# Performance work log

Hardware: AMD Instinct MI355X
Metric: run time of the kernel (lower is better)

The kernel has to match this reference:

```python
import jax, jax.numpy as jnp
import numpy as np
from jax.scipy.special import logsumexp

SIZE = 68          # DP length (self.size)
SSN = 8            # number of secondary-structure classes
C = SSN + 1        # states per step
S1 = SIZE + 1      # positions
BATCH = 256


def setup_inputs() -> dict:
    key = jax.random.key(0)
    k1, k2, k3, k4 = jax.random.split(key, 4)
    P = jax.random.normal(k1, (BATCH, 1, C, S1, S1), jnp.float32)
    Q = jax.random.normal(k2, (1, C, C, S1, S1), jnp.float32)
    pi = jax.random.normal(k3, (C,), jnp.float32)
    T = jnp.ones((1,), jnp.float32)
    ls = jax.random.randint(k4, (BATCH,), 0, S1, dtype=jnp.int32)
    return {"P": P, "Q": Q, "pi": pi, "T": T, "ls": ls}


def _max_alpha(P, Q, pi, T):
    # Viterbi-style max-plus recursion with logsumexp renormalization.
    b = P.shape[0]
    a0 = jnp.full((b, C, S1), -jnp.inf, P.dtype).at[:, :, 0].set(pi[None, :])
    n0 = logsumexp(a0, axis=(-1, -2), keepdims=True)      # (b,1,1)
    a0 = a0 - n0

    def step(carry, _):
        la, ln = carry                                    # (b,C,S1), (b,1,1)
        # broadcast sum over (b, c_prev, c_new, t_prev, t_new)
        M = P + T * Q + la[:, :, None, :, None]
        a = M.max(axis=(1, 3))                            # max over c_prev, t_prev -> (b,C,S1)
        n = ln + logsumexp(a, axis=(-1, -2), keepdims=True)
        a = a + ln - n
        return (a, n), (a, n)

    _, (a_seq, n_seq) = jax.lax.scan(step, (a0, n0), None, length=SIZE)
    a_all = jnp.concatenate([a0[None], a_seq], 0)          # (S1, b, C, S1) forward order
    n_all = jnp.concatenate([n0[None], n_seq], 0)          # (S1, b, 1, 1)
    # torch code stacks alpha REVERSED but norm in forward order, then adds
    alpha = a_all[::-1] + n_all
    return jnp.swapaxes(alpha, 0, 1)                       # (b, SIZE+1, C, S1)


def _backtrace(alpha, P, Q, T, ls):
    b = alpha.shape[0]
    Ps = P[:, 0]            # (b, C, S1, S1)
    Qs = Q[0]               # (C, C, S1, S1)
    bi = jnp.arange(b)
    c0 = jnp.full((b,), 3, jnp.int32)
    l0 = jnp.zeros((b,), jnp.int32)
    t0 = ls.astype(jnp.int32)

    def step(carry, a):
        c, l, t = carry
        Pterm = Ps[bi, c, :, t]                 # (b, S1)
        Qterm = Qs[c, :, :, t]                  # (b, C, S1)
        score = Pterm[:, None, :] + T * Qterm + a
        idx = jnp.argmax(score.reshape(b, -1), axis=-1).astype(jnp.int32)
        cn = idx // S1
        tn = idx % S1
        ln = tn - t
        return (cn, ln, tn), (cn, ln, tn)

    a_seq = jnp.swapaxes(alpha, 0, 1)[1:]       # (SIZE, b, C, S1)
    _, (cs, lss, ts) = jax.lax.scan(step, (c0, l0, t0), a_seq)
    c_all = jnp.concatenate([c0[None], cs], 0)[::-1]   # (SIZE+1, b)
    l_all = jnp.concatenate([l0[None], lss], 0)[::-1]
    t_all = jnp.concatenate([t0[None], ts], 0)[::-1]
    mp = jnp.swapaxes(jnp.stack([c_all, l_all, t_all], -1), 0, 1)  # (b, SIZE+1, 3)
    # shift length column: mp[:, :-1, 1] = mp[:, 1:, 1]; mp[:, -1, 1] = 0
    l_shift = jnp.concatenate([mp[:, 1:, 1], jnp.zeros((b, 1), jnp.int32)], 1)
    return mp.at[:, :, 1].set(l_shift)


def reference(P, Q, pi, T, ls):
    alpha = _max_alpha(P, Q, pi, T)
    max_pattern = _backtrace(alpha, P, Q, T, ls)
    return alpha, max_pattern
```

## Files before the change

### kernel.cpp

```cpp
#include <hip/hip_runtime.h>

#define C9     9
#define S1     69
#define JT     621
#define NBATCH 256
#define NSTEP  68
#define QJ     4761
#define QI     42849
#define BROW   42849
#define ALPHA_N (NBATCH*BROW)
#define QTFL   385664
#define NEGINF (-__builtin_inff())

typedef float float2u __attribute__((ext_vector_type(2), aligned(4)));

__global__ void qw_kernel(const float* __restrict__ Q, float* __restrict__ QW)
{
  const int bl = blockIdx.x;
  const int j = bl / S1, s = bl - j*S1;
  float* dst = QW + (size_t)bl*JT;
  const float* src = Q + (size_t)j*QJ + s*S1;
  for (int f = threadIdx.x; f < JT; f += 256){
    const int i = f / S1, t = f - i*S1;
    dst[f] = src[i*QJ + t];
  }
}

__global__ void qtrans_kernel(const float* __restrict__ Q, float* __restrict__ QT)
{
  __shared__ float tile[69*70];
  const int pl = blockIdx.x;
  const int c = pl / 9, i = pl - c*9;
  const float* src = Q + (size_t)pl*QJ;
  for (int f = threadIdx.x; f < QJ; f += 256){
    const int s = f / S1, t = f - s*S1;
    tile[s*70 + t] = src[f];
  }
  __syncthreads();
  float* dst = QT + (size_t)c*QI + i*S1;
  for (int f = threadIdx.x; f < QJ; f += 256){
    const int t = f / S1, s = f - t*S1;
    dst[t*JT + s] = tile[s*70 + t];
  }
}

template<int SI, int SS>
__device__ __forceinline__ float2u scan23(const float* __restrict__ qb,
                                          const float* __restrict__ pb,
                                          const float* __restrict__ laS,
                                          const float Tv)
{
#define LD(QB, S) { \
  const float* q_ = qb + (S)*SS; \
  _Pragma("unroll") \
  for (int i_ = 0; i_ < C9; ++i_) QB[i_] = *(const float2u*)(q_ + i_*SI); }
#define CM(QB, S) { \
  const float2u pv_ = *(const float2u*)(pb + (S)*S1); \
  float r0 = NEGINF, r1 = NEGINF; \
  _Pragma("unroll") \
  for (int i_ = 0; i_ < C9; ++i_){ \
    const float lv_ = laS[i_*72 + (S)]; \
    r0 = fmaxf(r0, fmaf(Tv, QB[i_].x, lv_)); \
    r1 = fmaxf(r1, fmaf(Tv, QB[i_].y, lv_)); \
  } \
  acc.x = fmaxf(acc.x, pv_.x + r0); \
  acc.y = fmaxf(acc.y, pv_.y + r1); }

  float2u acc; acc.x = acc.y = NEGINF;
  float2u qA[C9], qB[C9];
  LD(qA, 0)
  int s = 0;
  for (; s + 2 < 23; s += 2){
    LD(qB, s+1)
    CM(qA, s)
    LD(qA, s+2)
    CM(qB, s+1)
  }
  CM(qA, 22)
  return acc;
#undef LD
#undef CM
}

__global__ __launch_bounds__(1024) void mega_kernel(
    const float* __restrict__ P, const float* __restrict__ Q,
    const float* __restrict__ pi, const float* __restrict__ Tp,
    const int* __restrict__ ls, float* __restrict__ out,
    const float* __restrict__ QW, const float* __restrict__ QT, int wsmode)
{
  __shared__ __align__(16) float la[2][C9*72];
  __shared__ float part[2][315][3];
  __shared__ float red[16];
  __shared__ float m_sh[NSTEP+1], lse_sh[NSTEP+1], n_sh[NSTEP+1];
  __shared__ float sums_sh[NSTEP+1][5];
  __shared__ float sbest[16];
  __shared__ int   sidx[16];
  __shared__ int   sct[2];

  const int tid  = threadIdx.x;
  const int w    = tid >> 6;
  const int lane = tid & 63;
  const int b    = blockIdx.x;
  const bool act = tid < 945;
  const int gg   = act ? tid / 315 : 2;
  const int slot = act ? tid - gg*315 : 314;
  const int j    = slot / 35;
  const int tp   = slot - j*35;
  const bool own2 = (tp < 34);
  const int t0   = own2 ? 2*tp : 67;
  const int s_lo = gg*23;
  const float Tv = Tp[0];

  float* outb = out + (size_t)b*BROW;

  for (int e = tid; e < JT; e += 1024){
    const int i = e / S1, s = e - i*S1;
    const float v0 = (s == 0) ? pi[i] : NEGINF;
    outb[68*JT + e] = v0;
    la[0][i*72 + s] = v0;
  }
  if (tid == 0){
    float mx = pi[0];
    #pragma unroll
    for (int c = 1; c < C9; ++c) mx = fmaxf(mx, pi[c]);
    float sm = 0.f;
    #pragma unroll
    for (int c = 0; c < C9; ++c) sm += expf(pi[c] - mx);
    m_sh[0]   = mx;
    lse_sh[0] = mx + logf(sm);
  }
  __syncthreads();
  float mprev = m_sh[0];

  const bool useQW = (wsmode >= 1);
  const float* qw_b = QW + (size_t)j*QI + (size_t)s_lo*JT + t0;
  const float* qr_b = Q + (size_t)j*QJ + s_lo*S1 + t0;
  const float* p_b  = P + (size_t)(b*C9 + j)*QJ + s_lo*S1 + t0;

  int cur = 0;
  for (int k = 1; k <= NSTEP; ++k){
    const float* laS = la[cur] + s_lo;
    float2u acc;
    if (act){
      if (useQW) acc = scan23<S1, JT>(qw_b, p_b, laS, Tv);
      else       acc = scan23<QI, S1>(qr_b, p_b, laS, Tv);
      if (gg > 0){
        part[gg-1][slot][0] = acc.x;
        part[gg-1][slot][1] = acc.y;
      }
    }
    __syncthreads();

    float mval = NEGINF;
    float v0 = 0.f, v1 = 0.f;
    if (act && gg == 0){
      const float c0 = fmaxf(fmaxf(acc.x, part[0][slot][0]), part[1][slot][0]);
      const float c1 = fmaxf(fmaxf(acc.y, part[0][slot][1]), part[1][slot][1]);
      v0 = c0 - mprev;
      v1 = c1 - mprev;
      float* dst = outb + (size_t)(68-k)*JT + j*S1 + t0;
      if (own2){
        float2u vv; vv.x = v0; vv.y = v1;
        *(float2u*)dst = vv;
        la[cur^1][j*72 + t0]     = v0;
        la[cur^1][j*72 + t0 + 1] = v1;
        mval = fmaxf(v0, v1);
      } else {
        dst[1] = v1;
        la[cur^1][j*72 + 68] = v1;
        mval = v1;
      }
    }
    float mr = mval;
    #pragma unroll
    for (int o = 32; o >= 1; o >>= 1) mr = fmaxf(mr, __shfl_down(mr, o));
    if (lane == 0) red[w] = mr;
    __syncthreads();
    float mA = red[0];
    #pragma unroll
    for (int q = 1; q < 5; ++q) mA = fmaxf(mA, red[q]);
    if (act && gg == 0){
      float sv = own2 ? (expf(v0 - mA) + expf(v1 - mA)) : expf(v1 - mA);
      #pragma unroll
      for (int o = 32; o >= 1; o >>= 1) sv += __shfl_down(sv, o);
      if (lane == 0) sums_sh[k][w] = sv;
    }
    if (tid == 0) m_sh[k] = mA;
    mprev = mA;
    cur ^= 1;
  }
  __syncthreads();

  if (tid == 0){
    double dd = 0.0;
    for (int kk = 0; kk <= NSTEP; ++kk){
      float lse;
      if (kk == 0) lse = lse_sh[0];
      else {
        float S = sums_sh[kk][0];
        #pragma unroll
        for (int q = 1; q < 5; ++q) S += sums_sh[kk][q];
        lse = m_sh[kk] + logf(S);
      }
      lse_sh[kk] = lse;
      n_sh[kk] = (float)((double)lse + dd);
      dd += (double)m_sh[kk];
    }
  }
  __syncthreads();

  for (int K = 0; K <= NSTEP; ++K){
    const float Cst = n_sh[K] - lse_sh[68-K];
    for (int e = tid; e < JT; e += 1024){
      float* r = outb + (size_t)K*JT + e;
      *r = fmaxf(*r + Cst, -3.0e38f);
    }
  }
  __syncthreads();

  {
    int c = 3, t2 = ls[b];
    float* mpb = out + (size_t)ALPHA_N + (size_t)b*(69*3);
    if (tid == 0){
      mpb[68*3+0] = 3.f; mpb[68*3+1] = 0.f; mpb[68*3+2] = (float)t2;
      mpb[67*3+1] = 0.f;
    }
    const bool vok = tid < JT;
    const int etid = vok ? tid : 0;
    const int im = etid / S1;
    const int sm = etid - im*S1;
    float av = vok ? outb[1*JT + tid] : NEGINF;
    for (int r = 1; r <= NSTEP; ++r){
      float avn = NEGINF;
      if (r < NSTEP && vok) avn = outb[(size_t)(r+1)*JT + tid];
      float best = NEGINF; int bidx = 0x7fffffff;
      if (vok){
        float qv;
        if (wsmode >= 2)      qv = QT[(size_t)c*QI + (size_t)t2*JT + tid];
        else if (wsmode == 1) qv = QW[(size_t)c*QI + (size_t)sm*JT + im*S1 + t2];
        else                  qv = Q[(size_t)c*QI + (size_t)im*QJ + sm*S1 + t2];
        const float pv = P[(size_t)(b*C9 + c)*QJ + sm*S1 + t2];
        best = (pv + Tv*qv) + av;
        bidx = tid;
      }
      #pragma unroll
      for (int o = 32; o >= 1; o >>= 1){
        const float ov = __shfl_down(best, o); const int oi = __shfl_down(bidx, o);
        if (ov > best || (ov == best && oi < bidx)){ best = ov; bidx = oi; }
      }
      if (lane == 0){ sbest[w] = best; sidx[w] = bidx; }
      __syncthreads();
      if (tid == 0){
        float bb = sbest[0]; int bi = sidx[0];
        #pragma unroll
        for (int q = 1; q < 16; ++q)
          if (sbest[q] > bb || (sbest[q] == bb && sidx[q] < bi)){
            bb = sbest[q]; bi = sidx[q];
          }
        const int cn = bi / S1, tn = bi - cn*S1;
        mpb[(68-r)*3 + 0] = (float)cn;
        mpb[(68-r)*3 + 2] = (float)tn;
        if (r <= 67) mpb[(67-r)*3 + 1] = (float)(tn - t2);
        sct[0] = cn; sct[1] = tn;
      }
      __syncthreads();
      c = sct[0]; t2 = sct[1];
      av = avn;
    }
  }
}

extern "C" void kernel_launch(void* const* d_in, const int* in_sizes, int n_in,
                              void* d_out, int out_size, void* d_ws, size_t ws_size,
                              hipStream_t stream)
{
  const float* P  = (const float*)d_in[0];
  const float* Q  = (const float*)d_in[1];
  const float* pi = (const float*)d_in[2];
  const float* T  = (const float*)d_in[3];
  const int*   ls = (const int*)d_in[4];

  float* out = (float*)d_out;

  int wsmode = 0; float* QW = nullptr; float* QT = nullptr;
  if (ws_size >= (size_t)QTFL*4){ wsmode = 1; QW = (float*)d_ws; }
  if (ws_size >= (size_t)2*QTFL*4){ wsmode = 2; QT = (float*)d_ws + QTFL; }

  if (wsmode >= 1) qw_kernel<<<JT, 256, 0, stream>>>(Q, QW);
  if (wsmode >= 2) qtrans_kernel<<<81, 256, 0, stream>>>(Q, QT);
  mega_kernel<<<NBATCH, 1024, 0, stream>>>(P, Q, pi, T, ls, out, QW, QT, wsmode);
}
```

Before: 2.058 ms.

## Split DP scan over two thread groups and prefetch Q across steps

Each block now uses 704 threads, and the scan over previous positions is split into two groups of 35 positions instead of three groups of 23, so only one partial result buffer is merged per step. The step loop is unrolled by two with ping-pong register buffers, so the first Q slice for the next step is loaded before the barrier. A custom barrier waits only on LDS counters (lgkmcnt), letting global loads stay in flight across it. In exchange, each thread does a longer serial inner loop and the block has fewer waves to hide latency.

```diff
diff --git a/kernel.cpp b/kernel.cpp
--- a/kernel.cpp
+++ b/kernel.cpp
@@ -14,6 +14,14 @@
 
 typedef float float2u __attribute__((ext_vector_type(2), aligned(4)));
 
+__device__ __forceinline__ void barrier_lgkm()
+{
+  __builtin_amdgcn_sched_barrier(0);
+  asm volatile("s_waitcnt lgkmcnt(0)" ::: "memory");
+  __builtin_amdgcn_s_barrier();
+  __builtin_amdgcn_sched_barrier(0);
+}
+
 __global__ void qw_kernel(const float* __restrict__ Q, float* __restrict__ QW)
 {
   const int bl = blockIdx.x;
@@ -44,80 +52,42 @@
   }
 }
 
-template<int SI, int SS>
-__device__ __forceinline__ float2u scan23(const float* __restrict__ qb,
-                                          const float* __restrict__ pb,
-                                          const float* __restrict__ laS,
-                                          const float Tv)
-{
-#define LD(QB, S) { \
-  const float* q_ = qb + (S)*SS; \
-  _Pragma("unroll") \
-  for (int i_ = 0; i_ < C9; ++i_) QB[i_] = *(const float2u*)(q_ + i_*SI); }
-#define CM(QB, S) { \
-  const float2u pv_ = *(const float2u*)(pb + (S)*S1); \
-  float r0 = NEGINF, r1 = NEGINF; \
-  _Pragma("unroll") \
-  for (int i_ = 0; i_ < C9; ++i_){ \
-    const float lv_ = laS[i_*72 + (S)]; \
-    r0 = fmaxf(r0, fmaf(Tv, QB[i_].x, lv_)); \
-    r1 = fmaxf(r1, fmaf(Tv, QB[i_].y, lv_)); \
-  } \
-  acc.x = fmaxf(acc.x, pv_.x + r0); \
-  acc.y = fmaxf(acc.y, pv_.y + r1); }
-
-  float2u acc; acc.x = acc.y = NEGINF;
-  float2u qA[C9], qB[C9];
-  LD(qA, 0)
-  int s = 0;
-  for (; s + 2 < 23; s += 2){
-    LD(qB, s+1)
-    CM(qA, s)
-    LD(qA, s+2)
-    CM(qB, s+1)
-  }
-  CM(qA, 22)
-  return acc;
-#undef LD
-#undef CM
-}
-
-__global__ __launch_bounds__(1024) void mega_kernel(
+__global__ __launch_bounds__(704) void mega_kernel(
     const float* __restrict__ P, const float* __restrict__ Q,
     const float* __restrict__ pi, const float* __restrict__ Tp,
     const int* __restrict__ ls, float* __restrict__ out,
     const float* __restrict__ QW, const float* __restrict__ QT, int wsmode)
 {
   __shared__ __align__(16) float la[2][C9*72];
-  __shared__ float part[2][315][3];
-  __shared__ float red[16];
+  __shared__ float part[315][3];
+  __shared__ float red[11];
   __shared__ float m_sh[NSTEP+1], lse_sh[NSTEP+1], n_sh[NSTEP+1];
   __shared__ float sums_sh[NSTEP+1][5];
-  __shared__ float sbest[16];
-  __shared__ int   sidx[16];
+  __shared__ float sbest[11];
+  __shared__ int   sidx[11];
   __shared__ int   sct[2];
 
   const int tid  = threadIdx.x;
   const int w    = tid >> 6;
   const int lane = tid & 63;
   const int b    = blockIdx.x;
-  const bool act = tid < 945;
-  const int gg   = act ? tid / 315 : 2;
+  const bool act = tid < 630;
+  const int gg   = act ? tid / 315 : 1;
   const int slot = act ? tid - gg*315 : 314;
   const int j    = slot / 35;
   const int tp   = slot - j*35;
   const bool own2 = (tp < 34);
   const int t0   = own2 ? 2*tp : 67;
-  const int s_lo = gg*23;
+  const int s_lo = gg*34;
   const float Tv = Tp[0];
 
   float* outb = out + (size_t)b*BROW;
 
-  for (int e = tid; e < JT; e += 1024){
+  for (int e = tid; e < JT; e += 704){
     const int i = e / S1, s = e - i*S1;
-    const float v0 = (s == 0) ? pi[i] : NEGINF;
-    outb[68*JT + e] = v0;
-    la[0][i*72 + s] = v0;
+    const float v0i = (s == 0) ? pi[i] : NEGINF;
+    outb[68*JT + e] = v0i;
+    la[0][i*72 + s] = v0i;
   }
   if (tid == 0){
     float mx = pi[0];
@@ -133,62 +103,92 @@
   float mprev = m_sh[0];
 
   const bool useQW = (wsmode >= 1);
-  const float* qw_b = QW + (size_t)j*QI + (size_t)s_lo*JT + t0;
-  const float* qr_b = Q + (size_t)j*QJ + s_lo*S1 + t0;
-  const float* p_b  = P + (size_t)(b*C9 + j)*QJ + s_lo*S1 + t0;
-
-  int cur = 0;
-  for (int k = 1; k <= NSTEP; ++k){
-    const float* laS = la[cur] + s_lo;
-    float2u acc;
-    if (act){
-      if (useQW) acc = scan23<S1, JT>(qw_b, p_b, laS, Tv);
-      else       acc = scan23<QI, S1>(qr_b, p_b, laS, Tv);
-      if (gg > 0){
-        part[gg-1][slot][0] = acc.x;
-        part[gg-1][slot][1] = acc.y;
-      }
-    }
-    __syncthreads();
-
-    float mval = NEGINF;
-    float v0 = 0.f, v1 = 0.f;
-    if (act && gg == 0){
-      const float c0 = fmaxf(fmaxf(acc.x, part[0][slot][0]), part[1][slot][0]);
-      const float c1 = fmaxf(fmaxf(acc.y, part[0][slot][1]), part[1][slot][1]);
-      v0 = c0 - mprev;
-      v1 = c1 - mprev;
-      float* dst = outb + (size_t)(68-k)*JT + j*S1 + t0;
-      if (own2){
-        float2u vv; vv.x = v0; vv.y = v1;
-        *(float2u*)dst = vv;
-        la[cur^1][j*72 + t0]     = v0;
-        la[cur^1][j*72 + t0 + 1] = v1;
-        mval = fmaxf(v0, v1);
-      } else {
-        dst[1] = v1;
-        la[cur^1][j*72 + 68] = v1;
-        mval = v1;
-      }
-    }
-    float mr = mval;
-    #pragma unroll
-    for (int o = 32; o >= 1; o >>= 1) mr = fmaxf(mr, __shfl_down(mr, o));
-    if (lane == 0) red[w] = mr;
-    __syncthreads();
-    float mA = red[0];
-    #pragma unroll
-    for (int q = 1; q < 5; ++q) mA = fmaxf(mA, red[q]);
-    if (act && gg == 0){
-      float sv = own2 ? (expf(v0 - mA) + expf(v1 - mA)) : expf(v1 - mA);
-      #pragma unroll
-      for (int o = 32; o >= 1; o >>= 1) sv += __shfl_down(sv, o);
-      if (lane == 0) sums_sh[k][w] = sv;
-    }
-    if (tid == 0) m_sh[k] = mA;
-    mprev = mA;
-    cur ^= 1;
-  }
+  const float* qb = useQW ? (QW + (size_t)j*QI + (size_t)s_lo*JT + t0)
+                          : (Q  + (size_t)j*QJ + s_lo*S1 + t0);
+  const float* pb = P + (size_t)(b*C9 + j)*QJ + s_lo*S1 + t0;
+  float* la0 = la[0];
+  float* la1 = la[1];
+
+#define LDQ(B, PTR, SI) { \
+  _Pragma("unroll") \
+  for (int i_ = 0; i_ < C9; ++i_) B[i_] = *(const float2u*)((PTR) + i_*(SI)); }
+
+#define CMQ(B, PPTR, LC, IDX) { \
+  const float2u pv_ = *(const float2u*)(PPTR); \
+  float r0 = NEGINF, r1 = NEGINF; \
+  _Pragma("unroll") \
+  for (int i_ = 0; i_ < C9; ++i_){ \
+    const float lv_ = (LC)[i_*72 + (IDX)]; \
+    r0 = fmaxf(r0, fmaf(Tv, B[i_].x, lv_)); \
+    r1 = fmaxf(r1, fmaf(Tv, B[i_].y, lv_)); \
+  } \
+  acc.x = fmaxf(acc.x, pv_.x + r0); \
+  acc.y = fmaxf(acc.y, pv_.y + r1); }
+
+#define STEP(K, BE, BO, LAR, LAW, SI, SS) { \
+  float2u acc; acc.x = acc.y = NEGINF; \
+  if (act){ \
+    const float* qc = qb + (SS); \
+    const float* pc = pb; \
+    const float* lc = (LAR) + s_lo; \
+    for (int p_ = 0; p_ < 17; ++p_){ \
+      LDQ(BO, qc, SI) \
+      CMQ(BE, pc, lc, 0) \
+      LDQ(BE, qc + (SS), SI) \
+      CMQ(BO, pc + S1, lc, 1) \
+      qc += 2*(SS); pc += 2*S1; lc += 2; \
+    } \
+    LDQ(BO, qb, SI)                        \
+    CMQ(BE, pc, lc, 0)                     \
+    if (gg == 1){ part[slot][0] = acc.x; part[slot][1] = acc.y; } \
+  } \
+  barrier_lgkm();                          \
+  float mval = NEGINF; float v0 = 0.f, v1 = 0.f; \
+  if (act && gg == 0){ \
+    const float c0 = fmaxf(acc.x, part[slot][0]); \
+    const float c1 = fmaxf(acc.y, part[slot][1]); \
+    v0 = c0 - mprev; v1 = c1 - mprev; \
+    float* dst = outb + (size_t)(68-(K))*JT + j*S1 + t0; \
+    if (own2){ \
+      float2u vv; vv.x = v0; vv.y = v1; \
+      *(float2u*)dst = vv; \
+      (LAW)[j*72 + t0]     = v0; \
+      (LAW)[j*72 + t0 + 1] = v1; \
+      mval = fmaxf(v0, v1); \
+    } else { \
+      dst[1] = v1; \
+      (LAW)[j*72 + 68] = v1; \
+      mval = v1; \
+    } \
+  } \
+  float mr = mval; \
+  _Pragma("unroll") \
+  for (int o_ = 32; o_ >= 1; o_ >>= 1) mr = fmaxf(mr, __shfl_down(mr, o_)); \
+  if (lane == 0) red[w] = mr; \
+  barrier_lgkm();                          \
+  float mA = red[0]; \
+  _Pragma("unroll") \
+  for (int q_ = 1; q_ < 5; ++q_) mA = fmaxf(mA, red[q_]); \
+  float sv = 0.f; \
+  if (act && gg == 0) \
+    sv = own2 ? (expf(v0 - mA) + expf(v1 - mA)) : expf(v1 - mA); \
+  _Pragma("unroll") \
+  for (int o_ = 32; o_ >= 1; o_ >>= 1) sv += __shfl_down(sv, o_); \
+  if (lane == 0 && w < 5) sums_sh[K][w] = sv; \
+  if (tid == 0) m_sh[K] = mA; \
+  mprev = mA; }
+
+#define KLOOP(SI, SS) { \
+  float2u qE[C9], qO[C9]; \
+  if (act) LDQ(qE, qb, SI) \
+  for (int kk = 1; kk <= NSTEP; kk += 2){ \
+    STEP(kk,   qE, qO, la0, la1, SI, SS) \
+    STEP(kk+1, qO, qE, la1, la0, SI, SS) \
+  } }
+
+  if (useQW){ KLOOP(S1, JT) }
+  else      { KLOOP(QI, S1) }
+
   __syncthreads();
 
   if (tid == 0){
@@ -211,7 +211,7 @@
 
   for (int K = 0; K <= NSTEP; ++K){
     const float Cst = n_sh[K] - lse_sh[68-K];
-    for (int e = tid; e < JT; e += 1024){
+    for (int e = tid; e < JT; e += 704){
       float* r = outb + (size_t)K*JT + e;
       *r = fmaxf(*r + Cst, -3.0e38f);
     }
@@ -253,7 +253,7 @@
       if (tid == 0){
         float bb = sbest[0]; int bi = sidx[0];
         #pragma unroll
-        for (int q = 1; q < 16; ++q)
+        for (int q = 1; q < 11; ++q)
           if (sbest[q] > bb || (sbest[q] == bb && sidx[q] < bi)){
             bb = sbest[q]; bi = sidx[q];
           }
@@ -288,5 +288,5 @@
 
   if (wsmode >= 1) qw_kernel<<<JT, 256, 0, stream>>>(Q, QW);
   if (wsmode >= 2) qtrans_kernel<<<81, 256, 0, stream>>>(Q, QT);
-  mega_kernel<<<NBATCH, 1024, 0, stream>>>(P, Q, pi, T, ls, out, QW, QT, wsmode);
-}
+  mega_kernel<<<NBATCH, 704, 0, stream>>>(P, Q, pi, T, ls, out, QW, QT, wsmode);
+}
```

After: 2.111 ms. 1.03x slower.

## Split each 4-batch group across 4 cooperating blocks with global-memory step exchange

Applied to the files above, without the earlier changes.

The forward max-plus recursion is reorganized so that each group of 4 blocks handles 4 batch elements jointly. Each block owns a slice of the output time positions for all 4 batches, so every Q load is reused across 4 batches. The blocks exchange per-step column results and maxima through a global scratch buffer, synchronized with atomic flag counters and spin-waits. A fallback kernel with 704 threads covers the case of small workspace, and barriers now wait only on LDS counters. The aim is to cut per-block Q traffic and shorten the serial work per step. In exchange there is inter-block spin synchronization every step, which depends on all 4 blocks of a group being resident at the same time.

```diff
diff --git a/kernel.cpp b/kernel.cpp
--- a/kernel.cpp
+++ b/kernel.cpp
@@ -10,9 +10,23 @@
 #define BROW   42849
 #define ALPHA_N (NBATCH*BROW)
 #define QTFL   385664
+#define XCSTR  672
+#define XCFL   (64*2*4*XCSTR)
+#define FLAGN  4608
 #define NEGINF (-__builtin_inff())
 
-typedef float float2u __attribute__((ext_vector_type(2), aligned(4)));
+typedef float float2u  __attribute__((ext_vector_type(2), aligned(4)));
+typedef float float4a  __attribute__((ext_vector_type(4), aligned(16)));
+
+#define AGENT __HIP_MEMORY_SCOPE_AGENT
+
+__device__ __forceinline__ void barrier_lgkm()
+{
+  __builtin_amdgcn_sched_barrier(0);
+  asm volatile("s_waitcnt lgkmcnt(0)" ::: "memory");
+  __builtin_amdgcn_s_barrier();
+  __builtin_amdgcn_sched_barrier(0);
+}
 
 __global__ void qw_kernel(const float* __restrict__ Q, float* __restrict__ QW)
 {
@@ -44,80 +58,61 @@
   }
 }
 
-template<int SI, int SS>
-__device__ __forceinline__ float2u scan23(const float* __restrict__ qb,
-                                          const float* __restrict__ pb,
-                                          const float* __restrict__ laS,
-                                          const float Tv)
+__global__ void zf_kernel(unsigned* __restrict__ f)
 {
-#define LD(QB, S) { \
-  const float* q_ = qb + (S)*SS; \
-  _Pragma("unroll") \
-  for (int i_ = 0; i_ < C9; ++i_) QB[i_] = *(const float2u*)(q_ + i_*SI); }
-#define CM(QB, S) { \
-  const float2u pv_ = *(const float2u*)(pb + (S)*S1); \
-  float r0 = NEGINF, r1 = NEGINF; \
-  _Pragma("unroll") \
-  for (int i_ = 0; i_ < C9; ++i_){ \
-    const float lv_ = laS[i_*72 + (S)]; \
-    r0 = fmaxf(r0, fmaf(Tv, QB[i_].x, lv_)); \
-    r1 = fmaxf(r1, fmaf(Tv, QB[i_].y, lv_)); \
-  } \
-  acc.x = fmaxf(acc.x, pv_.x + r0); \
-  acc.y = fmaxf(acc.y, pv_.y + r1); }
-
-  float2u acc; acc.x = acc.y = NEGINF;
-  float2u qA[C9], qB[C9];
-  LD(qA, 0)
-  int s = 0;
-  for (; s + 2 < 23; s += 2){
-    LD(qB, s+1)
-    CM(qA, s)
-    LD(qA, s+2)
-    CM(qB, s+1)
-  }
-  CM(qA, 22)
-  return acc;
-#undef LD
-#undef CM
+  const int i = blockIdx.x*256 + threadIdx.x;
+  if (i < FLAGN) __hip_atomic_store(&f[i], 0u, __ATOMIC_RELAXED, AGENT);
 }
 
-__global__ __launch_bounds__(1024) void mega_kernel(
+__global__ __launch_bounds__(704) void mega_group(
     const float* __restrict__ P, const float* __restrict__ Q,
     const float* __restrict__ pi, const float* __restrict__ Tp,
     const int* __restrict__ ls, float* __restrict__ out,
-    const float* __restrict__ QW, const float* __restrict__ QT, int wsmode)
+    const float* __restrict__ QW, const float* __restrict__ QT,
+    float* __restrict__ XC, unsigned* __restrict__ FLAGS, int qtmode)
 {
-  __shared__ __align__(16) float la[2][C9*72];
-  __shared__ float part[2][315][3];
-  __shared__ float red[16];
-  __shared__ float m_sh[NSTEP+1], lse_sh[NSTEP+1], n_sh[NSTEP+1];
-  __shared__ float sums_sh[NSTEP+1][5];
-  __shared__ float sbest[16];
-  __shared__ int   sidx[16];
+  __shared__ __align__(16) float la4[C9*70*4];
+  __shared__ __align__(16) float part[7][81][8];
+  __shared__ float cbuf[4][624];
+  __shared__ float msh[NSTEP+1][4];
+  __shared__ float sums_sh[NSTEP+1][11][4];
+  __shared__ float mpart[2][4];
+  __shared__ float lse_sh[NSTEP+1], n_sh[NSTEP+1];
+  __shared__ float lse0_sh;
+  __shared__ float sbest[11];
+  __shared__ int   sidx[11];
   __shared__ int   sct[2];
 
   const int tid  = threadIdx.x;
-  const int w    = tid >> 6;
-  const int lane = tid & 63;
-  const int b    = blockIdx.x;
-  const bool act = tid < 945;
-  const int gg   = act ? tid / 315 : 2;
-  const int slot = act ? tid - gg*315 : 314;
-  const int j    = slot / 35;
-  const int tp   = slot - j*35;
-  const bool own2 = (tp < 34);
-  const int t0   = own2 ? 2*tp : 67;
-  const int s_lo = gg*23;
+  const int w    = tid >> 6, lane = tid & 63;
+  const int g    = blockIdx.x >> 2, h = blockIdx.x & 3;
+  const int Th   = h ? 17 : 18;
+  const int Bh   = h ? (18 + 17*(h-1)) : 0;
+  const bool act = tid < 648;
+  const int sg   = act ? tid / 81 : 7;
+  const int slot = act ? tid - sg*81 : 80;
+  const int j    = slot / 9;
+  const int tp   = slot - j*9;
+  const bool own2 = (2*tp + 1 < Th);
+  const int tl0  = own2 ? 2*tp : (Th-2);
+  const int tg0  = Bh + tl0;
+  const int Ws   = (sg < 7) ? 9 : 6;
+  const int s_lo = sg*9;
   const float Tv = Tp[0];
-
-  float* outb = out + (size_t)b*BROW;
-
-  for (int e = tid; e < JT; e += 1024){
-    const int i = e / S1, s = e - i*S1;
-    const float v0 = (s == 0) ? pi[i] : NEGINF;
-    outb[68*JT + e] = v0;
-    la[0][i*72 + s] = v0;
+  const int bb   = 4*g + h;
+  unsigned* flg  = FLAGS + g*72;
+
+  for (int e = tid; e < JT; e += 704){
+    const int ii = e / 69, ss = e - ii*69;
+    const float v0 = (ss == 0) ? pi[ii] : NEGINF;
+    float4a vv; vv.x = vv.y = vv.z = vv.w = v0;
+    *(float4a*)(&la4[(ii*70 + ss)*4]) = vv;
+  }
+  for (int idx = tid; idx < 4*9*Th; idx += 704){
+    const int m = idx / (9*Th); const int rem = idx - m*(9*Th);
+    const int jj = rem / Th;    const int tl = rem - jj*Th;
+    const int t = Bh + tl;
+    out[(size_t)(4*g+m)*BROW + 68*JT + jj*69 + t] = (t == 0) ? pi[jj] : NEGINF;
   }
   if (tid == 0){
     float mx = pi[0];
@@ -126,92 +121,223 @@
     float sm = 0.f;
     #pragma unroll
     for (int c = 0; c < C9; ++c) sm += expf(pi[c] - mx);
-    m_sh[0]   = mx;
-    lse_sh[0] = mx + logf(sm);
-  }
-  __syncthreads();
-  float mprev = m_sh[0];
-
-  const bool useQW = (wsmode >= 1);
-  const float* qw_b = QW + (size_t)j*QI + (size_t)s_lo*JT + t0;
-  const float* qr_b = Q + (size_t)j*QJ + s_lo*S1 + t0;
-  const float* p_b  = P + (size_t)(b*C9 + j)*QJ + s_lo*S1 + t0;
-
-  int cur = 0;
+    #pragma unroll
+    for (int m = 0; m < 4; ++m) msh[0][m] = mx;
+    lse0_sh = mx + logf(sm);
+  }
+  __syncthreads();
+  float mprev0 = msh[0][0], mprev1 = msh[0][1], mprev2 = msh[0][2], mprev3 = msh[0][3];
+
+  const float* qb  = QW + (size_t)j*QI + (size_t)s_lo*JT + tg0;
+  const float* pb0 = P + (size_t)((4*g+0)*C9 + j)*QJ + s_lo*S1 + tg0;
+  const float* pb1 = pb0 + QI;
+  const float* pb2 = pb1 + QI;
+  const float* pb3 = pb2 + QI;
+
+#define GLD(B, D) { \
+  const float* q_ = qb + (size_t)(D)*JT; \
+  _Pragma("unroll") \
+  for (int i_ = 0; i_ < 9; ++i_) B[i_] = *(const float2u*)(q_ + i_*S1); }
+
+#define GCM(B, D) { \
+  const int sa_ = s_lo + (D); \
+  const float2u pv0 = *(const float2u*)(pb0 + (D)*S1); \
+  const float2u pv1 = *(const float2u*)(pb1 + (D)*S1); \
+  const float2u pv2 = *(const float2u*)(pb2 + (D)*S1); \
+  const float2u pv3 = *(const float2u*)(pb3 + (D)*S1); \
+  float2u r0, r1, r2, r3; \
+  r0.x=r0.y=r1.x=r1.y=r2.x=r2.y=r3.x=r3.y=NEGINF; \
+  _Pragma("unroll") \
+  for (int i_ = 0; i_ < 9; ++i_){ \
+    const float4a lv = *(const float4a*)(&la4[(i_*70 + sa_)*4]); \
+    const float qx = B[i_].x, qy = B[i_].y; \
+    r0.x=fmaxf(r0.x,fmaf(Tv,qx,lv.x)); r0.y=fmaxf(r0.y,fmaf(Tv,qy,lv.x)); \
+    r1.x=fmaxf(r1.x,fmaf(Tv,qx,lv.y)); r1.y=fmaxf(r1.y,fmaf(Tv,qy,lv.y)); \
+    r2.x=fmaxf(r2.x,fmaf(Tv,qx,lv.z)); r2.y=fmaxf(r2.y,fmaf(Tv,qy,lv.z)); \
+    r3.x=fmaxf(r3.x,fmaf(Tv,qx,lv.w)); r3.y=fmaxf(r3.y,fmaf(Tv,qy,lv.w)); \
+  } \
+  acc0.x=fmaxf(acc0.x,pv0.x+r0.x); acc0.y=fmaxf(acc0.y,pv0.y+r0.y); \
+  acc1.x=fmaxf(acc1.x,pv1.x+r1.x); acc1.y=fmaxf(acc1.y,pv1.y+r1.y); \
+  acc2.x=fmaxf(acc2.x,pv2.x+r2.x); acc2.y=fmaxf(acc2.y,pv2.y+r2.y); \
+  acc3.x=fmaxf(acc3.x,pv3.x+r3.x); acc3.y=fmaxf(acc3.y,pv3.y+r3.y); }
+
   for (int k = 1; k <= NSTEP; ++k){
-    const float* laS = la[cur] + s_lo;
-    float2u acc;
+    float2u acc0, acc1, acc2, acc3;
+    acc0.x=acc0.y=acc1.x=acc1.y=acc2.x=acc2.y=acc3.x=acc3.y=NEGINF;
     if (act){
-      if (useQW) acc = scan23<S1, JT>(qw_b, p_b, laS, Tv);
-      else       acc = scan23<QI, S1>(qr_b, p_b, laS, Tv);
-      if (gg > 0){
-        part[gg-1][slot][0] = acc.x;
-        part[gg-1][slot][1] = acc.y;
-      }
+      float2u qA[9], qB[9];
+      GLD(qA, 0)
+      int d = 0;
+      for (; d + 2 < Ws; d += 2){
+        GLD(qB, d+1)  GCM(qA, d)  GLD(qA, d+2)  GCM(qB, d+1)
+      }
+      if (d + 1 < Ws){ GLD(qB, d+1) GCM(qA, d) GCM(qB, d+1) }
+      else { GCM(qA, d) }
+      if (sg > 0){
+        float4a u0; u0.x=acc0.x; u0.y=acc0.y; u0.z=acc1.x; u0.w=acc1.y;
+        float4a u1; u1.x=acc2.x; u1.y=acc2.y; u1.z=acc3.x; u1.w=acc3.y;
+        *(float4a*)(&part[sg-1][slot][0]) = u0;
+        *(float4a*)(&part[sg-1][slot][4]) = u1;
+      }
+    }
+    barrier_lgkm();
+
+    float* xcm = XC + (size_t)(((g*2 + (k&1))*4) + h)*XCSTR;
+    float cm0=NEGINF, cm1=NEGINF, cm2=NEGINF, cm3=NEGINF;
+    if (act && sg == 0){
+      float2u c0=acc0, c1=acc1, c2=acc2, c3=acc3;
+      #pragma unroll
+      for (int gq = 0; gq < 7; ++gq){
+        const float4a t0 = *(const float4a*)(&part[gq][slot][0]);
+        const float4a t1 = *(const float4a*)(&part[gq][slot][4]);
+        c0.x=fmaxf(c0.x,t0.x); c0.y=fmaxf(c0.y,t0.y);
+        c1.x=fmaxf(c1.x,t0.z); c1.y=fmaxf(c1.y,t0.w);
+        c2.x=fmaxf(c2.x,t1.x); c2.y=fmaxf(c2.y,t1.y);
+        c3.x=fmaxf(c3.x,t1.z); c3.y=fmaxf(c3.y,t1.w);
+      }
+      const int colbase = j*69 + tg0;
+      const int pubj = j*Th + tl0;
+#define EMIT(MB, CC, MPREV, CM) { \
+      const float vx = CC.x - (MPREV), vy = CC.y - (MPREV); \
+      float* dst = out + (size_t)(4*g+MB)*BROW + (size_t)(68-k)*JT + colbase; \
+      const int pb_ = MB*9*Th + pubj; \
+      if (own2){ \
+        float2u vv; vv.x=vx; vv.y=vy; *(float2u*)dst = vv; \
+        cbuf[MB][colbase] = CC.x; cbuf[MB][colbase+1] = CC.y; \
+        __hip_atomic_store(xcm + pb_,     CC.x, __ATOMIC_RELAXED, AGENT); \
+        __hip_atomic_store(xcm + pb_ + 1, CC.y, __ATOMIC_RELAXED, AGENT); \
+        CM = fmaxf(CC.x, CC.y); \
+      } else { \
+        dst[1] = vy; \
+        cbuf[MB][colbase+1] = CC.y; \
+        __hip_atomic_store(xcm + pb_ + 1, CC.y, __ATOMIC_RELAXED, AGENT); \
+        CM = CC.y; \
+      } }
+      EMIT(0, c0, mprev0, cm0)
+      EMIT(1, c1, mprev1, cm1)
+      EMIT(2, c2, mprev2, cm2)
+      EMIT(3, c3, mprev3, cm3)
+#undef EMIT
+    }
+    float mv0 = cm0, mv1 = cm1, mv2 = cm2, mv3 = cm3;
+    #pragma unroll
+    for (int o = 32; o >= 1; o >>= 1){
+      mv0 = fmaxf(mv0, __shfl_down(mv0, o));
+      mv1 = fmaxf(mv1, __shfl_down(mv1, o));
+      mv2 = fmaxf(mv2, __shfl_down(mv2, o));
+      mv3 = fmaxf(mv3, __shfl_down(mv3, o));
+    }
+    if (lane == 0 && w < 2){
+      mpart[w][0]=mv0; mpart[w][1]=mv1; mpart[w][2]=mv2; mpart[w][3]=mv3;
     }
     __syncthreads();
 
-    float mval = NEGINF;
-    float v0 = 0.f, v1 = 0.f;
-    if (act && gg == 0){
-      const float c0 = fmaxf(fmaxf(acc.x, part[0][slot][0]), part[1][slot][0]);
-      const float c1 = fmaxf(fmaxf(acc.y, part[0][slot][1]), part[1][slot][1]);
-      v0 = c0 - mprev;
-      v1 = c1 - mprev;
-      float* dst = outb + (size_t)(68-k)*JT + j*S1 + t0;
-      if (own2){
-        float2u vv; vv.x = v0; vv.y = v1;
-        *(float2u*)dst = vv;
-        la[cur^1][j*72 + t0]     = v0;
-        la[cur^1][j*72 + t0 + 1] = v1;
-        mval = fmaxf(v0, v1);
-      } else {
-        dst[1] = v1;
-        la[cur^1][j*72 + 68] = v1;
-        mval = v1;
-      }
-    }
-    float mr = mval;
-    #pragma unroll
-    for (int o = 32; o >= 1; o >>= 1) mr = fmaxf(mr, __shfl_down(mr, o));
-    if (lane == 0) red[w] = mr;
-    __syncthreads();
-    float mA = red[0];
-    #pragma unroll
-    for (int q = 1; q < 5; ++q) mA = fmaxf(mA, red[q]);
-    if (act && gg == 0){
-      float sv = own2 ? (expf(v0 - mA) + expf(v1 - mA)) : expf(v1 - mA);
+    unsigned* flagk = flg + k;
+    if (tid == 0){
       #pragma unroll
-      for (int o = 32; o >= 1; o >>= 1) sv += __shfl_down(sv, o);
-      if (lane == 0) sums_sh[k][w] = sv;
-    }
-    if (tid == 0) m_sh[k] = mA;
-    mprev = mA;
-    cur ^= 1;
-  }
-  __syncthreads();
-
+      for (int m = 0; m < 4; ++m){
+        const float mm = fmaxf(mpart[0][m], mpart[1][m]);
+        __hip_atomic_store(xcm + 656 + m, mm, __ATOMIC_RELAXED, AGENT);
+      }
+      asm volatile("s_waitcnt vmcnt(0)" ::: "memory");
+      __hip_atomic_fetch_add(flagk, 1u, __ATOMIC_RELEASE, AGENT);
+      int it = 0;
+      while (__hip_atomic_load(flagk, __ATOMIC_RELAXED, AGENT) < 4u){
+        __builtin_amdgcn_s_sleep(2);
+        if (++it > 3000000) break;
+      }
+      (void)__hip_atomic_load(flagk, __ATOMIC_ACQUIRE, AGENT);
+      float q0=NEGINF, q1=NEGINF, q2=NEGINF, q3=NEGINF;
+      #pragma unroll
+      for (int hh = 0; hh < 4; ++hh){
+        const float* src = XC + (size_t)(((g*2 + (k&1))*4) + hh)*XCSTR + 656;
+        q0 = fmaxf(q0, __hip_atomic_load(src + 0, __ATOMIC_RELAXED, AGENT));
+        q1 = fmaxf(q1, __hip_atomic_load(src + 1, __ATOMIC_RELAXED, AGENT));
+        q2 = fmaxf(q2, __hip_atomic_load(src + 2, __ATOMIC_RELAXED, AGENT));
+        q3 = fmaxf(q3, __hip_atomic_load(src + 3, __ATOMIC_RELAXED, AGENT));
+      }
+      msh[k][0] = q0 - mprev0;  msh[k][1] = q1 - mprev1;
+      msh[k][2] = q2 - mprev2;  msh[k][3] = q3 - mprev3;
+    }
+    barrier_lgkm();
+
+    #pragma unroll
+    for (int hh = 0; hh < 4; ++hh){
+      if (hh == h) continue;
+      const int Whh = hh ? 17 : 18;
+      const int Bhh = hh ? (18 + 17*(hh-1)) : 0;
+      const int n = 36*Whh;
+      if (tid < n){
+        const float* src = XC + (size_t)(((g*2 + (k&1))*4) + hh)*XCSTR;
+        const int m = tid / (9*Whh); const int rem = tid - m*(9*Whh);
+        const int jj = rem / Whh;    const int tl = rem - jj*Whh;
+        cbuf[m][jj*69 + Bhh + tl] = __hip_atomic_load(src + tid, __ATOMIC_RELAXED, AGENT);
+      }
+    }
+    barrier_lgkm();
+
+    const float mk0 = msh[k][0], mk1 = msh[k][1], mk2 = msh[k][2], mk3 = msh[k][3];
+    float s0 = 0.f, s1 = 0.f, s2 = 0.f, s3 = 0.f;
+    if (tid < JT){
+      const int ii = tid / 69, ss = tid - ii*69;
+      const float v0 = cbuf[0][tid] - mprev0;
+      const float v1 = cbuf[1][tid] - mprev1;
+      const float v2 = cbuf[2][tid] - mprev2;
+      const float v3 = cbuf[3][tid] - mprev3;
+      float4a vv; vv.x=v0; vv.y=v1; vv.z=v2; vv.w=v3;
+      *(float4a*)(&la4[(ii*70 + ss)*4]) = vv;
+      s0 = expf(v0 - mk0); s1 = expf(v1 - mk1);
+      s2 = expf(v2 - mk2); s3 = expf(v3 - mk3);
+    }
+    #pragma unroll
+    for (int o = 32; o >= 1; o >>= 1){
+      s0 += __shfl_down(s0, o); s1 += __shfl_down(s1, o);
+      s2 += __shfl_down(s2, o); s3 += __shfl_down(s3, o);
+    }
+    if (lane == 0){
+      sums_sh[k][w][0]=s0; sums_sh[k][w][1]=s1;
+      sums_sh[k][w][2]=s2; sums_sh[k][w][3]=s3;
+    }
+    mprev0 = mk0; mprev1 = mk1; mprev2 = mk2; mprev3 = mk3;
+    barrier_lgkm();
+  }
+
+  __syncthreads();
+  if (tid == 0){
+    __threadfence();
+    unsigned* flagF = flg + 69;
+    __hip_atomic_fetch_add(flagF, 1u, __ATOMIC_RELEASE, AGENT);
+    int it = 0;
+    while (__hip_atomic_load(flagF, __ATOMIC_RELAXED, AGENT) < 4u){
+      __builtin_amdgcn_s_sleep(2);
+      if (++it > 3000000) break;
+    }
+    (void)__hip_atomic_load(flagF, __ATOMIC_ACQUIRE, AGENT);
+  }
+  __syncthreads();
+
+  float* outb = out + (size_t)bb*BROW;
   if (tid == 0){
     double dd = 0.0;
     for (int kk = 0; kk <= NSTEP; ++kk){
       float lse;
-      if (kk == 0) lse = lse_sh[0];
+      if (kk == 0) lse = lse0_sh;
       else {
-        float S = sums_sh[kk][0];
+        float S = 0.f;
         #pragma unroll
-        for (int q = 1; q < 5; ++q) S += sums_sh[kk][q];
-        lse = m_sh[kk] + logf(S);
+        for (int q = 0; q < 11; ++q) S += sums_sh[kk][q][h];
+        lse = msh[kk][h] + logf(S);
       }
       lse_sh[kk] = lse;
       n_sh[kk] = (float)((double)lse + dd);
-      dd += (double)m_sh[kk];
+      dd += (double)msh[kk][h];
     }
   }
   __syncthreads();
 
   for (int K = 0; K <= NSTEP; ++K){
     const float Cst = n_sh[K] - lse_sh[68-K];
-    for (int e = tid; e < JT; e += 1024){
+    for (int e = tid; e < JT; e += 704){
       float* r = outb + (size_t)K*JT + e;
       *r = fmaxf(*r + Cst, -3.0e38f);
     }
@@ -219,8 +345,8 @@
   __syncthreads();
 
   {
-    int c = 3, t2 = ls[b];
-    float* mpb = out + (size_t)ALPHA_N + (size_t)b*(69*3);
+    int c = 3, t2 = ls[bb];
+    float* mpb = out + (size_t)ALPHA_N + (size_t)bb*(69*3);
     if (tid == 0){
       mpb[68*3+0] = 3.f; mpb[68*3+1] = 0.f; mpb[68*3+2] = (float)t2;
       mpb[67*3+1] = 0.f;
@@ -236,10 +362,9 @@
       float best = NEGINF; int bidx = 0x7fffffff;
       if (vok){
         float qv;
-        if (wsmode >= 2)      qv = QT[(size_t)c*QI + (size_t)t2*JT + tid];
-        else if (wsmode == 1) qv = QW[(size_t)c*QI + (size_t)sm*JT + im*S1 + t2];
-        else                  qv = Q[(size_t)c*QI + (size_t)im*QJ + sm*S1 + t2];
-        const float pv = P[(size_t)(b*C9 + c)*QJ + sm*S1 + t2];
+        if (qtmode >= 2) qv = QT[(size_t)c*QI + (size_t)t2*JT + tid];
+        else             qv = QW[(size_t)c*QI + (size_t)sm*JT + im*S1 + t2];
+        const float pv = P[(size_t)(bb*C9 + c)*QJ + sm*S1 + t2];
         best = (pv + Tv*qv) + av;
         bidx = tid;
       }
@@ -251,12 +376,186 @@
       if (lane == 0){ sbest[w] = best; sidx[w] = bidx; }
       __syncthreads();
       if (tid == 0){
-        float bb = sbest[0]; int bi = sidx[0];
+        float bbv = sbest[0]; int bi = sidx[0];
         #pragma unroll
-        for (int q = 1; q < 16; ++q)
-          if (sbest[q] > bb || (sbest[q] == bb && sidx[q] < bi)){
-            bb = sbest[q]; bi = sidx[q];
+        for (int q = 1; q < 11; ++q)
+          if (sbest[q] > bbv || (sbest[q] == bbv && sidx[q] < bi)){
+            bbv = sbest[q]; bi = sidx[q];
           }
+        const int cn = bi / S1, tn = bi - cn*S1;
+        mpb[(68-r)*3 + 0] = (float)cn;
+        mpb[(68-r)*3 + 2] = (float)tn;
+        if (r <= 67) mpb[(67-r)*3 + 1] = (float)(tn - t2);
+        sct[0] = cn; sct[1] = tn;
+      }
+      __syncthreads();
+      c = sct[0]; t2 = sct[1];
+      av = avn;
+    }
+  }
+}
+
+__global__ __launch_bounds__(704) void mega_fb(
+    const float* __restrict__ P, const float* __restrict__ Q,
+    const float* __restrict__ pi, const float* __restrict__ Tp,
+    const int* __restrict__ ls, float* __restrict__ out,
+    const float* __restrict__ QW, int wsmode)
+{
+  __shared__ __align__(16) float la[2][C9*72];
+  __shared__ float part[315][3];
+  __shared__ float red[11];
+  __shared__ float m_sh[NSTEP+1], lse_sh[NSTEP+1], n_sh[NSTEP+1];
+  __shared__ float sums_sh[NSTEP+1][5];
+  __shared__ float sbest[11];
+  __shared__ int   sidx[11];
+  __shared__ int   sct[2];
+
+  const int tid = threadIdx.x, w = tid>>6, lane = tid&63, b = blockIdx.x;
+  const bool act = tid < 630;
+  const int gg = act ? tid/315 : 1;
+  const int slot = act ? tid - gg*315 : 314;
+  const int j = slot/35, tp = slot - j*35;
+  const bool own2 = (tp < 34);
+  const int t0 = own2 ? 2*tp : 67;
+  const int s_lo = gg*34;
+  const float Tv = Tp[0];
+  float* outb = out + (size_t)b*BROW;
+
+  for (int e = tid; e < JT; e += 704){
+    const int i = e/S1, s = e - i*S1;
+    const float v0i = (s==0)? pi[i] : NEGINF;
+    outb[68*JT + e] = v0i;
+    la[0][i*72 + s] = v0i;
+  }
+  if (tid == 0){
+    float mx = pi[0];
+    #pragma unroll
+    for (int c = 1; c < C9; ++c) mx = fmaxf(mx, pi[c]);
+    float sm = 0.f;
+    #pragma unroll
+    for (int c = 0; c < C9; ++c) sm += expf(pi[c]-mx);
+    m_sh[0] = mx;  lse_sh[0] = mx + logf(sm);
+  }
+  __syncthreads();
+  float mprev = m_sh[0];
+  const bool useQW = (wsmode >= 1);
+  const float* qb = useQW ? (QW + (size_t)j*QI + (size_t)s_lo*JT + t0)
+                          : (Q  + (size_t)j*QJ + s_lo*S1 + t0);
+  const float* pb = P + (size_t)(b*C9 + j)*QJ + s_lo*S1 + t0;
+  const int SIv = useQW ? S1 : QI;
+  const int SSv = useQW ? JT : S1;
+
+  for (int k = 1; k <= NSTEP; ++k){
+    const float* laC = la[(k-1)&1];
+    float accx = NEGINF, accy = NEGINF;
+    if (act){
+      float2u qA[9], qB[9];
+      #define FLD(B, D) { const float* q_ = qb + (size_t)(D)*SSv; \
+        _Pragma("unroll") for (int i_=0;i_<9;++i_) B[i_] = *(const float2u*)(q_ + i_*SIv); }
+      #define FCM(B, D) { const float2u pv_ = *(const float2u*)(pb + (D)*S1); \
+        float r0=NEGINF, r1=NEGINF; \
+        _Pragma("unroll") for (int i_=0;i_<9;++i_){ \
+          const float lv_ = laC[i_*72 + s_lo + (D)]; \
+          r0 = fmaxf(r0, fmaf(Tv, B[i_].x, lv_)); \
+          r1 = fmaxf(r1, fmaf(Tv, B[i_].y, lv_)); } \
+        accx = fmaxf(accx, pv_.x + r0); accy = fmaxf(accy, pv_.y + r1); }
+      FLD(qA, 0)
+      int d = 0;
+      for (; d + 2 < 35; d += 2){ FLD(qB,d+1) FCM(qA,d) FLD(qA,d+2) FCM(qB,d+1) }
+      FCM(qA, 34)
+      #undef FLD
+      #undef FCM
+      if (gg == 1){ part[slot][0] = accx; part[slot][1] = accy; }
+    }
+    barrier_lgkm();
+    float mval = NEGINF, v0 = 0.f, v1 = 0.f;
+    if (act && gg == 0){
+      v0 = fmaxf(accx, part[slot][0]) - mprev;
+      v1 = fmaxf(accy, part[slot][1]) - mprev;
+      float* dst = outb + (size_t)(68-k)*JT + j*S1 + t0;
+      if (own2){
+        float2u vv; vv.x=v0; vv.y=v1; *(float2u*)dst = vv;
+        la[k&1][j*72 + t0] = v0; la[k&1][j*72 + t0 + 1] = v1;
+        mval = fmaxf(v0, v1);
+      } else { dst[1] = v1; la[k&1][j*72 + 68] = v1; mval = v1; }
+    }
+    float mr = mval;
+    #pragma unroll
+    for (int o = 32; o >= 1; o >>= 1) mr = fmaxf(mr, __shfl_down(mr, o));
+    if (lane == 0) red[w] = mr;
+    barrier_lgkm();
+    float mA = red[0];
+    #pragma unroll
+    for (int q = 1; q < 5; ++q) mA = fmaxf(mA, red[q]);
+    float sv = 0.f;
+    if (act && gg == 0) sv = own2 ? (expf(v0-mA)+expf(v1-mA)) : expf(v1-mA);
+    #pragma unroll
+    for (int o = 32; o >= 1; o >>= 1) sv += __shfl_down(sv, o);
+    if (lane == 0 && w < 5) sums_sh[k][w] = sv;
+    if (tid == 0) m_sh[k] = mA;
+    mprev = mA;
+    barrier_lgkm();
+  }
+  __syncthreads();
+  if (tid == 0){
+    double dd = 0.0;
+    for (int kk = 0; kk <= NSTEP; ++kk){
+      float lse;
+      if (kk == 0) lse = lse_sh[0];
+      else {
+        float S = sums_sh[kk][0];
+        #pragma unroll
+        for (int q = 1; q < 5; ++q) S += sums_sh[kk][q];
+        lse = m_sh[kk] + logf(S);
+      }
+      lse_sh[kk] = lse;
+      n_sh[kk] = (float)((double)lse + dd);
+      dd += (double)m_sh[kk];
+    }
+  }
+  __syncthreads();
+  for (int K = 0; K <= NSTEP; ++K){
+    const float Cst = n_sh[K] - lse_sh[68-K];
+    for (int e = tid; e < JT; e += 704){
+      float* r = outb + (size_t)K*JT + e;
+      *r = fmaxf(*r + Cst, -3.0e38f);
+    }
+  }
+  __syncthreads();
+  {
+    int c = 3, t2 = ls[b];
+    float* mpb = out + (size_t)ALPHA_N + (size_t)b*(69*3);
+    if (tid == 0){
+      mpb[68*3+0] = 3.f; mpb[68*3+1] = 0.f; mpb[68*3+2] = (float)t2;
+      mpb[67*3+1] = 0.f;
+    }
+    const bool vok = tid < JT;
+    const int etid = vok ? tid : 0;
+    const int im = etid / S1, sm = etid - im*S1;
+    float av = vok ? outb[1*JT + tid] : NEGINF;
+    for (int r = 1; r <= NSTEP; ++r){
+      float avn = NEGINF;
+      if (r < NSTEP && vok) avn = outb[(size_t)(r+1)*JT + tid];
+      float best = NEGINF; int bidx = 0x7fffffff;
+      if (vok){
+        float qv;
+        if (wsmode >= 1) qv = QW[(size_t)c*QI + (size_t)sm*JT + im*S1 + t2];
+        else             qv = Q[(size_t)c*QI + (size_t)im*QJ + sm*S1 + t2];
+        const float pv = P[(size_t)(b*C9 + c)*QJ + sm*S1 + t2];
+        best = (pv + Tv*qv) + av; bidx = tid;
+      }
+      #pragma unroll
+      for (int o = 32; o >= 1; o >>= 1){
+        const float ov = __shfl_down(best, o); const int oi = __shfl_down(bidx, o);
+        if (ov > best || (ov == best && oi < bidx)){ best = ov; bidx = oi; }
+      }
+      if (lane == 0){ sbest[w] = best; sidx[w] = bidx; }
+      __syncthreads();
+      if (tid == 0){
+        float bbv = sbest[0]; int bi = sidx[0];
+        #pragma unroll
+        for (int q = 1; q < 11; ++q)
+          if (sbest[q] > bbv || (sbest[q] == bbv && sidx[q] < bi)){ bbv = sbest[q]; bi = sidx[q]; }
         const int cn = bi / S1, tn = bi - cn*S1;
         mpb[(68-r)*3 + 0] = (float)cn;
         mpb[(68-r)*3 + 2] = (float)tn;
@@ -279,14 +578,27 @@
   const float* pi = (const float*)d_in[2];
   const float* T  = (const float*)d_in[3];
   const int*   ls = (const int*)d_in[4];
-
   float* out = (float*)d_out;
-
-  int wsmode = 0; float* QW = nullptr; float* QT = nullptr;
-  if (ws_size >= (size_t)QTFL*4){ wsmode = 1; QW = (float*)d_ws; }
-  if (ws_size >= (size_t)2*QTFL*4){ wsmode = 2; QT = (float*)d_ws + QTFL; }
-
-  if (wsmode >= 1) qw_kernel<<<JT, 256, 0, stream>>>(Q, QW);
-  if (wsmode >= 2) qtrans_kernel<<<81, 256, 0, stream>>>(Q, QT);
-  mega_kernel<<<NBATCH, 1024, 0, stream>>>(P, Q, pi, T, ls, out, QW, QT, wsmode);
+  float* wsf = (float*)d_ws;
+
+  const size_t need_base = (size_t)(QTFL + XCFL + FLAGN)*4;
+  const size_t need_full = need_base + (size_t)QTFL*4;
+
+  if (ws_size >= need_base){
+    float*    QW    = wsf;
+    float*    XC    = wsf + QTFL;
+    unsigned* FLAGS = (unsigned*)(wsf + QTFL + XCFL);
+    float*    QT    = nullptr;
+    int qtmode = 1;
+    if (ws_size >= need_full){ QT = wsf + QTFL + XCFL + FLAGN; qtmode = 2; }
+    zf_kernel<<<18, 256, 0, stream>>>(FLAGS);
+    qw_kernel<<<JT, 256, 0, stream>>>(Q, QW);
+    if (qtmode >= 2) qtrans_kernel<<<81, 256, 0, stream>>>(Q, QT);
+    mega_group<<<NBATCH, 704, 0, stream>>>(P, Q, pi, T, ls, out, QW, QT, XC, FLAGS, qtmode);
+  } else {
+    int wsmode = 0; float* QW = nullptr;
+    if (ws_size >= (size_t)QTFL*4){ wsmode = 1; QW = wsf; }
+    if (wsmode >= 1) qw_kernel<<<JT, 256, 0, stream>>>(Q, QW);
+    mega_fb<<<NBATCH, 704, 0, stream>>>(P, Q, pi, T, ls, out, QW, wsmode);
+  }
 }
```

Result: slower. 2.345 ms (+14.0%).
